# Optimization experiments

Measured on AMD Instinct MI355X. Metric: run time of the kernel, lower is better.

## Reference

```python
import jax, jax.numpy as jnp
import numpy as np

B, C, H, W = 4, 256, 64, 64
CK = C // 8  # key/query channels = 32


def setup_inputs() -> dict:
    key = jax.random.key(0)
    ks = jax.random.split(key, 5)
    s = 0.02
    return {
        "x": jax.random.normal(ks[0], (B, C, H, W), dtype=jnp.float32),
        "fw": jax.random.normal(ks[1], (CK, C), dtype=jnp.float32) * s,
        "fb": jnp.zeros((CK,), dtype=jnp.float32),
        "gw": jax.random.normal(ks[2], (CK, C), dtype=jnp.float32) * s,
        "gb": jnp.zeros((CK,), dtype=jnp.float32),
        "hw": jax.random.normal(ks[3], (C, C), dtype=jnp.float32) * s,
        "hb": jnp.zeros((C,), dtype=jnp.float32),
        "gamma": jax.random.normal(ks[4], (1,), dtype=jnp.float32),
    }


def reference(x, fw, fb, gw, gb, hw, hb, gamma):
    b, c, h, w = x.shape
    n = h * w
    xf = x.reshape(b, c, n)  # [B, C, N]
    # 1x1 convs == channel matmuls
    f = jnp.einsum('oc,bcn->bon', fw, xf) + fb[None, :, None]  # [B, CK, N]
    g = jnp.einsum('oc,bcn->bon', gw, xf) + gb[None, :, None]  # [B, CK, N]
    hv = jnp.einsum('oc,bcn->bon', hw, xf) + hb[None, :, None]  # [B, C, N]
    # attention[b,i,j] = sum_k f[b,k,i] * g[b,k,j]; softmax over j (no scaling, as in source)
    attention = jax.nn.softmax(jnp.einsum('bki,bkj->bij', f, g), axis=-1)  # [B, N, N]
    # torch.bmm(h, attention): out[b,c,m] = sum_j hv[b,c,j] * attention[b,j,m]
    sa = jnp.einsum('bcj,bjm->bcm', hv, attention).reshape(b, c, h, w)
    return gamma * sa + x
```

## Files before the change

### kernel.cpp

```cpp
#include <hip/hip_runtime.h>


typedef __bf16 bf16x4 __attribute__((ext_vector_type(4)));
typedef __bf16 bf16x8 __attribute__((ext_vector_type(8)));
typedef float  f32x4  __attribute__((ext_vector_type(4)));

static __device__ __forceinline__ bf16x8 cvt8(f32x4 lo, f32x4 hi) {
  bf16x8 r;
  r[0]=(__bf16)lo[0]; r[1]=(__bf16)lo[1]; r[2]=(__bf16)lo[2]; r[3]=(__bf16)lo[3];
  r[4]=(__bf16)hi[0]; r[5]=(__bf16)hi[1]; r[6]=(__bf16)hi[2]; r[7]=(__bf16)hi[3];
  return r;
}

__global__ __launch_bounds__(256, 2) void k_proj(
    const float* __restrict__ fw, const float* __restrict__ gw,
    const float* __restrict__ hw, const float* __restrict__ x,
    const float* __restrict__ fb, const float* __restrict__ gb,
    const float* __restrict__ hb,
    __bf16* __restrict__ gT, __bf16* __restrict__ fF, __bf16* __restrict__ hvF) {
  __shared__ __bf16 Bs[2][32][40];
  const int bid = blockIdx.x;
  const int b = (bid & 7) >> 1;
  const int n0 = (((bid >> 3) << 1) | (bid & 1)) * 32;
  const int t = threadIdx.x, mq = t >> 6, lane = t & 63, r16 = lane & 15, h = lane >> 4;
  const float* xb = x + (size_t)b * (256 * 4096);
  const float* Wp[5];
  #pragma unroll
  for (int mt = 0; mt < 5; ++mt) {
    const int wrow = mq * 80 + mt * 16 + r16;
    Wp[mt] = wrow < 32 ? (fw + wrow * 256)
           : wrow < 64 ? (gw + (wrow - 32) * 256)
                       : (hw + (wrow - 64) * 256);
  }
  const int kk = t >> 3, nc = (t & 7) * 4;
  f32x4 acc[5][2] = {};
  {
    f32x4 xv = *(const f32x4*)&xb[(size_t)kk * 4096 + n0 + nc];
    Bs[0][nc + 0][kk] = (__bf16)xv[0]; Bs[0][nc + 1][kk] = (__bf16)xv[1];
    Bs[0][nc + 2][kk] = (__bf16)xv[2]; Bs[0][nc + 3][kk] = (__bf16)xv[3];
  }
  __syncthreads();
  for (int ks = 0; ks < 8; ++ks) {
    const int cur = ks & 1;
    f32x4 xn;
    if (ks < 7) xn = *(const f32x4*)&xb[(size_t)((ks + 1) * 32 + kk) * 4096 + n0 + nc];
    bf16x8 bf0 = *(const bf16x8*)&Bs[cur][r16][h * 8];
    bf16x8 bf1 = *(const bf16x8*)&Bs[cur][16 + r16][h * 8];
    #pragma unroll
    for (int mt = 0; mt < 5; ++mt) {
      f32x4 wlo = *(const f32x4*)(Wp[mt] + ks * 32 + h * 8);
      f32x4 whi = *(const f32x4*)(Wp[mt] + ks * 32 + h * 8 + 4);
      bf16x8 af = cvt8(wlo, whi);
      acc[mt][0] = __builtin_amdgcn_mfma_f32_16x16x32_bf16(af, bf0, acc[mt][0], 0, 0, 0);
      acc[mt][1] = __builtin_amdgcn_mfma_f32_16x16x32_bf16(af, bf1, acc[mt][1], 0, 0, 0);
    }
    if (ks < 7) {
      const int nxt = cur ^ 1;
      Bs[nxt][nc + 0][kk] = (__bf16)xn[0]; Bs[nxt][nc + 1][kk] = (__bf16)xn[1];
      Bs[nxt][nc + 2][kk] = (__bf16)xn[2]; Bs[nxt][nc + 3][kk] = (__bf16)xn[3];
    }
    __syncthreads();
  }
  #pragma unroll
  for (int mt = 0; mt < 5; ++mt) {
    #pragma unroll
    for (int nt = 0; nt < 2; ++nt) {
      const int nn = n0 + nt * 16 + r16;
      const int fragn = (((b * 64 + (nn >> 6)) * 2 + ((nn >> 5) & 1)) * 2 + ((nn >> 4) & 1));
      const int jt2 = nn >> 6, jh2 = (nn >> 5) & 1;
      const int h2 = (nn >> 2) & 3, s2 = (nn >> 4) & 1, b2 = nn & 3;
      #pragma unroll
      for (int r = 0; r < 4; ++r) {
        const int row = mq * 80 + mt * 16 + h * 4 + r;
        const float bias = row < 32 ? fb[row] : (row < 64 ? gb[row - 32] : hb[row - 64]);
        float val = acc[mt][nt][r] + bias;
        if (row < 32) {
          val *= 1.44269504089f;
          const size_t off = (size_t)fragn * 512
            + (size_t)(((row >> 3) * 16 + (nn & 15)) * 8) + (row & 7);
          fF[off] = (__bf16)val;
        } else if (row < 64) {
          gT[((size_t)b * 4096 + nn) * 32 + (row - 32)] = (__bf16)val;
        } else {
          const int c = row - 64;
          const size_t off = (size_t)b * 1048576
            + (size_t)(32 * jt2 + 8 * (c >> 6) + 4 * jh2 + ((c >> 4) & 3)) * 512
            + (h2 * 16 + (c & 15)) * 8 + s2 * 4 + b2;
          hvF[off] = (__bf16)val;
        }
      }
    }
  }
}

__global__ __launch_bounds__(256) void k_pass1(const __bf16* __restrict__ gT,
                                               const __bf16* __restrict__ fF,
                                               float* __restrict__ Lp) {
  const int bid = blockIdx.x;
  const int b = (bid & 7) >> 1;
  const int sub = ((bid >> 3) << 1) | (bid & 1);
  const int ms = sub >> 6, ib = sub & 63;
  const int w = threadIdx.x >> 6, lane = threadIdx.x & 63, r16 = lane & 15, h = lane >> 4;
  const __bf16* gb_ = gT + (size_t)b * 4096 * 32;
  const int fragn = ((b * 64 + ib) * 2 + (w >> 1)) * 2 + (w & 1);
  const bf16x8 afrag = *(const bf16x8*)(fF + (size_t)fragn * 512 + lane * 8);
  const f32x4 zero = {};
  float ls0 = 0.f, ls1 = 0.f, ls2 = 0.f, ls3 = 0.f;
  for (int mt = 0; mt < 64; mt += 2) {
    const int mb = ms * 1024 + mt * 16;
    bf16x8 g0 = *(const bf16x8*)(gb_ + (size_t)(mb + r16) * 32 + h * 8);
    bf16x8 g1 = *(const bf16x8*)(gb_ + (size_t)(mb + 16 + r16) * 32 + h * 8);
    f32x4 d0 = __builtin_amdgcn_mfma_f32_16x16x32_bf16(afrag, g0, zero, 0, 0, 0);
    f32x4 d1 = __builtin_amdgcn_mfma_f32_16x16x32_bf16(afrag, g1, zero, 0, 0, 0);
    ls0 += __builtin_amdgcn_exp2f(d0[0]) + __builtin_amdgcn_exp2f(d1[0]);
    ls1 += __builtin_amdgcn_exp2f(d0[1]) + __builtin_amdgcn_exp2f(d1[1]);
    ls2 += __builtin_amdgcn_exp2f(d0[2]) + __builtin_amdgcn_exp2f(d1[2]);
    ls3 += __builtin_amdgcn_exp2f(d0[3]) + __builtin_amdgcn_exp2f(d1[3]);
  }
  #pragma unroll
  for (int off = 1; off < 16; off <<= 1) {
    ls0 += __shfl_xor(ls0, off); ls1 += __shfl_xor(ls1, off);
    ls2 += __shfl_xor(ls2, off); ls3 += __shfl_xor(ls3, off);
  }
  if (r16 == 0) {
    f32x4 o = {ls0, ls1, ls2, ls3};
    *(f32x4*)&Lp[(size_t)(b * 4 + ms) * 4096 + ib * 64 + w * 16 + h * 4] = o;
  }
}

__global__ __launch_bounds__(256) void k_wdiv(__bf16* __restrict__ hvF,
                                              const float* __restrict__ Lp) {
  const int bid = blockIdx.x;
  const int b = (bid & 7) >> 1;
  const int chunk = ((bid >> 3) << 1) | (bid & 1);
  const int t = threadIdx.x;
  const int o = chunk * 8192 + t * 32;
  const int frag = o >> 9;
  const int jh = (frag >> 2) & 1;
  const int jt = frag >> 5;
  const int l0 = (o >> 3) & 63;
  const int jb = jt * 64 + jh * 32 + ((l0 >> 4) << 2);
  const float* lp = Lp + (size_t)b * 16384 + jb;
  f32x4 La = *(const f32x4*)lp;
  La += *(const f32x4*)(lp + 4096);
  La += *(const f32x4*)(lp + 8192);
  La += *(const f32x4*)(lp + 12288);
  f32x4 Lb = *(const f32x4*)(lp + 16);
  Lb += *(const f32x4*)(lp + 16 + 4096);
  Lb += *(const f32x4*)(lp + 16 + 8192);
  Lb += *(const f32x4*)(lp + 16 + 12288);
  __bf16* p = hvF + (size_t)b * 1048576 + o;
  bf16x4 in[8];
  #pragma unroll
  for (int k = 0; k < 8; ++k) in[k] = *(const bf16x4*)(p + k * 4);
  #pragma unroll
  for (int k = 0; k < 8; ++k) {
    const f32x4 L = (k & 1) ? Lb : La;
    bf16x4 ov;
    #pragma unroll
    for (int bb = 0; bb < 4; ++bb)
      ov[bb] = (__bf16)((float)in[k][bb] / L[bb]);
    *(bf16x4*)(p + k * 4) = ov;
  }
}

__global__ __launch_bounds__(256, 2) void k_pass2(const __bf16* __restrict__ gT,
    const __bf16* __restrict__ fF, const __bf16* __restrict__ wF,
    const float* __restrict__ x, const float* __restrict__ gamma,
    float* __restrict__ out) {
  __shared__ float red[8192];
  const int bid = blockIdx.x;
  const int b = (bid & 7) >> 1;
  const int sub = ((bid >> 3) << 1) | (bid & 1);
  const int ch = sub >> 6;
  const int mblk = sub & 63;
  const int t = threadIdx.x, w = t >> 6, lane = t & 63, r16 = lane & 15, h = lane >> 4;
  const int jh = w & 1, msub = w >> 1;
  const int mbase = mblk * 64 + msub * 32;
  const __bf16* gb_ = gT + (size_t)b * 4096 * 32;
  const bf16x8 gf0 = *(const bf16x8*)(gb_ + (size_t)(mbase + r16) * 32 + h * 8);
  const bf16x8 gf1 = *(const bf16x8*)(gb_ + (size_t)(mbase + 16 + r16) * 32 + h * 8);
  const __bf16* wbase = wF + (size_t)b * 1048576 + lane * 8;
  size_t wo[8];
  #pragma unroll
  for (int ctt = 0; ctt < 8; ++ctt)
    wo[ctt] = (size_t)(8 * (2 * ch + (ctt >> 2)) + 4 * jh + (ctt & 3)) * 512;
  const __bf16* fbase = fF + ((size_t)(b * 64) * 2 + jh) * 2 * 512 + lane * 8;
  const f32x4 zero = {};

  f32x4 acc[8] = {};
  f32x4 acc2[8] = {};

  bf16x8 a0 = *(const bf16x8*)(wbase + wo[0]);
  bf16x8 a1 = *(const bf16x8*)(wbase + wo[1]);
  bf16x8 a2 = *(const bf16x8*)(wbase + wo[2]);
  bf16x8 a3 = *(const bf16x8*)(wbase + wo[3]);
  bf16x8 a4 = *(const bf16x8*)(wbase + wo[4]);
  bf16x8 a5 = *(const bf16x8*)(wbase + wo[5]);
  bf16x8 a6 = *(const bf16x8*)(wbase + wo[6]);
  bf16x8 a7 = *(const bf16x8*)(wbase + wo[7]);
  bf16x8 fq0 = *(const bf16x8*)(fbase);
  bf16x8 fq1 = *(const bf16x8*)(fbase + 512);
  bf16x8 ef0, ef1;
  {
    f32x4 d0 = __builtin_amdgcn_mfma_f32_16x16x32_bf16(fq0, gf0, zero, 0, 0, 0);
    f32x4 d1 = __builtin_amdgcn_mfma_f32_16x16x32_bf16(fq1, gf0, zero, 0, 0, 0);
    f32x4 d2 = __builtin_amdgcn_mfma_f32_16x16x32_bf16(fq0, gf1, zero, 0, 0, 0);
    f32x4 d3 = __builtin_amdgcn_mfma_f32_16x16x32_bf16(fq1, gf1, zero, 0, 0, 0);
    #pragma unroll
    for (int r = 0; r < 4; ++r) {
      ef0[r]     = (__bf16)__builtin_amdgcn_exp2f(d0[r]);
      ef0[4 + r] = (__bf16)__builtin_amdgcn_exp2f(d1[r]);
      ef1[r]     = (__bf16)__builtin_amdgcn_exp2f(d2[r]);
      ef1[4 + r] = (__bf16)__builtin_amdgcn_exp2f(d3[r]);
    }
  }
  fq0 = *(const bf16x8*)(fbase + 2048);
  fq1 = *(const bf16x8*)(fbase + 2048 + 512);

  for (int it = 0; it < 64; ++it) {
    bf16x8 pa0, pa1, pa2, pa3, pa4, pa5, pa6, pa7, nf0, nf1;
    if (it < 63) {
      const __bf16* wn = wbase + (size_t)(it + 1) * 16384;
      pa0 = *(const bf16x8*)(wn + wo[0]);
      pa1 = *(const bf16x8*)(wn + wo[1]);
      pa2 = *(const bf16x8*)(wn + wo[2]);
      pa3 = *(const bf16x8*)(wn + wo[3]);
      pa4 = *(const bf16x8*)(wn + wo[4]);
      pa5 = *(const bf16x8*)(wn + wo[5]);
      pa6 = *(const bf16x8*)(wn + wo[6]);
      pa7 = *(const bf16x8*)(wn + wo[7]);
      const __bf16* fn = fbase + (size_t)(it + 2) * 2048;
      nf0 = *(const bf16x8*)(fn);
      nf1 = *(const bf16x8*)(fn + 512);
    }
    f32x4 d0, d1, d2, d3;
    if (it < 63) {
      d0 = __builtin_amdgcn_mfma_f32_16x16x32_bf16(fq0, gf0, zero, 0, 0, 0);
      d1 = __builtin_amdgcn_mfma_f32_16x16x32_bf16(fq1, gf0, zero, 0, 0, 0);
      d2 = __builtin_amdgcn_mfma_f32_16x16x32_bf16(fq0, gf1, zero, 0, 0, 0);
      d3 = __builtin_amdgcn_mfma_f32_16x16x32_bf16(fq1, gf1, zero, 0, 0, 0);
    }
    acc[0]  = __builtin_amdgcn_mfma_f32_16x16x32_bf16(a0, ef0, acc[0],  0, 0, 0);
    acc2[0] = __builtin_amdgcn_mfma_f32_16x16x32_bf16(a0, ef1, acc2[0], 0, 0, 0);
    acc[1]  = __builtin_amdgcn_mfma_f32_16x16x32_bf16(a1, ef0, acc[1],  0, 0, 0);
    acc2[1] = __builtin_amdgcn_mfma_f32_16x16x32_bf16(a1, ef1, acc2[1], 0, 0, 0);
    acc[2]  = __builtin_amdgcn_mfma_f32_16x16x32_bf16(a2, ef0, acc[2],  0, 0, 0);
    acc2[2] = __builtin_amdgcn_mfma_f32_16x16x32_bf16(a2, ef1, acc2[2], 0, 0, 0);
    acc[3]  = __builtin_amdgcn_mfma_f32_16x16x32_bf16(a3, ef0, acc[3],  0, 0, 0);
    acc2[3] = __builtin_amdgcn_mfma_f32_16x16x32_bf16(a3, ef1, acc2[3], 0, 0, 0);
    acc[4]  = __builtin_amdgcn_mfma_f32_16x16x32_bf16(a4, ef0, acc[4],  0, 0, 0);
    acc2[4] = __builtin_amdgcn_mfma_f32_16x16x32_bf16(a4, ef1, acc2[4], 0, 0, 0);
    acc[5]  = __builtin_amdgcn_mfma_f32_16x16x32_bf16(a5, ef0, acc[5],  0, 0, 0);
    acc2[5] = __builtin_amdgcn_mfma_f32_16x16x32_bf16(a5, ef1, acc2[5], 0, 0, 0);
    acc[6]  = __builtin_amdgcn_mfma_f32_16x16x32_bf16(a6, ef0, acc[6],  0, 0, 0);
    acc2[6] = __builtin_amdgcn_mfma_f32_16x16x32_bf16(a6, ef1, acc2[6], 0, 0, 0);
    acc[7]  = __builtin_amdgcn_mfma_f32_16x16x32_bf16(a7, ef0, acc[7],  0, 0, 0);
    acc2[7] = __builtin_amdgcn_mfma_f32_16x16x32_bf16(a7, ef1, acc2[7], 0, 0, 0);
    if (it < 63) {
      #pragma unroll
      for (int r = 0; r < 4; ++r) {
        ef0[r]     = (__bf16)__builtin_amdgcn_exp2f(d0[r]);
        ef0[4 + r] = (__bf16)__builtin_amdgcn_exp2f(d1[r]);
        ef1[r]     = (__bf16)__builtin_amdgcn_exp2f(d2[r]);
        ef1[4 + r] = (__bf16)__builtin_amdgcn_exp2f(d3[r]);
      }
      a0 = pa0; a1 = pa1; a2 = pa2; a3 = pa3;
      a4 = pa4; a5 = pa5; a6 = pa6; a7 = pa7;
      fq0 = nf0; fq1 = nf1;
    }
  }

  __syncthreads();
  const int region = msub * 4096;
  if (jh == 1) {
    #pragma unroll
    for (int ct = 0; ct < 8; ++ct) {
      *(f32x4*)&red[region + ((ct * 2 + 0) * 64 + lane) * 4] = acc[ct];
      *(f32x4*)&red[region + ((ct * 2 + 1) * 64 + lane) * 4] = acc2[ct];
    }
  }
  __syncthreads();
  if (jh == 0) {
    const float gm = gamma[0];
    const float* xb = x + (size_t)b * (256 * 4096);
    float* ob = out + (size_t)b * (256 * 4096);
    #pragma unroll
    for (int ct = 0; ct < 8; ++ct) {
      #pragma unroll
      for (int mt = 0; mt < 2; ++mt) {
        f32x4 o = *(const f32x4*)&red[region + ((ct * 2 + mt) * 64 + lane) * 4];
        o += (mt == 0) ? acc[ct] : acc2[ct];
        #pragma unroll
        for (int r = 0; r < 4; ++r) {
          const int c = ch * 128 + ct * 16 + h * 4 + r;
          const size_t idx = (size_t)c * 4096 + (mbase + mt * 16 + r16);
          ob[idx] = gm * o[r] + xb[idx];
        }
      }
    }
  }
}

extern "C" void kernel_launch(void* const* d_in, const int* in_sizes, int n_in,
                              void* d_out, int out_size, void* d_ws, size_t ws_size,
                              hipStream_t stream) {
  const float* x     = (const float*)d_in[0];
  const float* fw    = (const float*)d_in[1];
  const float* fb    = (const float*)d_in[2];
  const float* gw    = (const float*)d_in[3];
  const float* gb    = (const float*)d_in[4];
  const float* hw    = (const float*)d_in[5];
  const float* hb    = (const float*)d_in[6];
  const float* gamma = (const float*)d_in[7];
  float* out = (float*)d_out;

  char* wsb = (char*)d_ws;
  __bf16* gT  = (__bf16*)(wsb);
  __bf16* fF  = (__bf16*)(wsb + 1048576);
  __bf16* hvF = (__bf16*)(wsb + 2097152);
  float*  Lp  = (float*) (wsb + 10485760);

  k_proj<<<dim3(512), dim3(256), 0, stream>>>(fw, gw, hw, x, fb, gb, hb, gT, fF, hvF);
  k_pass1<<<dim3(1024), dim3(256), 0, stream>>>(gT, fF, Lp);
  k_wdiv<<<dim3(512), dim3(256), 0, stream>>>(hvF, Lp);
  k_pass2<<<dim3(512), dim3(256), 0, stream>>>(gT, fF, hvF, x, gamma, out);
}
```

Before: 107.9 us.

## Halve pass2 query tile per wave, double grid, drop software prefetch

```diff
diff --git a/kernel.cpp b/kernel.cpp
--- a/kernel.cpp
+++ b/kernel.cpp
@@ -164,121 +164,65 @@
   }
 }
 
-__global__ __launch_bounds__(256, 2) void k_pass2(const __bf16* __restrict__ gT,
+__global__ __launch_bounds__(256, 4) void k_pass2(const __bf16* __restrict__ gT,
     const __bf16* __restrict__ fF, const __bf16* __restrict__ wF,
     const float* __restrict__ x, const float* __restrict__ gamma,
     float* __restrict__ out) {
-  __shared__ float red[8192];
+  __shared__ float red[4096];
   const int bid = blockIdx.x;
   const int b = (bid & 7) >> 1;
   const int sub = ((bid >> 3) << 1) | (bid & 1);
-  const int ch = sub >> 6;
-  const int mblk = sub & 63;
+  const int ch = sub >> 7;
+  const int mblk = sub & 127;
   const int t = threadIdx.x, w = t >> 6, lane = t & 63, r16 = lane & 15, h = lane >> 4;
   const int jh = w & 1, msub = w >> 1;
-  const int mbase = mblk * 64 + msub * 32;
+  const int mbase = mblk * 32 + msub * 16;
   const __bf16* gb_ = gT + (size_t)b * 4096 * 32;
-  const bf16x8 gf0 = *(const bf16x8*)(gb_ + (size_t)(mbase + r16) * 32 + h * 8);
-  const bf16x8 gf1 = *(const bf16x8*)(gb_ + (size_t)(mbase + 16 + r16) * 32 + h * 8);
-  const __bf16* wbase = wF + (size_t)b * 1048576 + lane * 8;
-  size_t wo[8];
-  #pragma unroll
-  for (int ctt = 0; ctt < 8; ++ctt)
-    wo[ctt] = (size_t)(8 * (2 * ch + (ctt >> 2)) + 4 * jh + (ctt & 3)) * 512;
+  const bf16x8 gf = *(const bf16x8*)(gb_ + (size_t)(mbase + r16) * 32 + h * 8);
+  const __bf16* wbase = wF + (size_t)b * 1048576
+                      + (size_t)(8 * (2 * ch) + 4 * jh) * 512 + lane * 8;
   const __bf16* fbase = fF + ((size_t)(b * 64) * 2 + jh) * 2 * 512 + lane * 8;
   const f32x4 zero = {};
 
   f32x4 acc[8] = {};
-  f32x4 acc2[8] = {};
-
-  bf16x8 a0 = *(const bf16x8*)(wbase + wo[0]);
-  bf16x8 a1 = *(const bf16x8*)(wbase + wo[1]);
-  bf16x8 a2 = *(const bf16x8*)(wbase + wo[2]);
-  bf16x8 a3 = *(const bf16x8*)(wbase + wo[3]);
-  bf16x8 a4 = *(const bf16x8*)(wbase + wo[4]);
-  bf16x8 a5 = *(const bf16x8*)(wbase + wo[5]);
-  bf16x8 a6 = *(const bf16x8*)(wbase + wo[6]);
-  bf16x8 a7 = *(const bf16x8*)(wbase + wo[7]);
-  bf16x8 fq0 = *(const bf16x8*)(fbase);
-  bf16x8 fq1 = *(const bf16x8*)(fbase + 512);
-  bf16x8 ef0, ef1;
-  {
-    f32x4 d0 = __builtin_amdgcn_mfma_f32_16x16x32_bf16(fq0, gf0, zero, 0, 0, 0);
-    f32x4 d1 = __builtin_amdgcn_mfma_f32_16x16x32_bf16(fq1, gf0, zero, 0, 0, 0);
-    f32x4 d2 = __builtin_amdgcn_mfma_f32_16x16x32_bf16(fq0, gf1, zero, 0, 0, 0);
-    f32x4 d3 = __builtin_amdgcn_mfma_f32_16x16x32_bf16(fq1, gf1, zero, 0, 0, 0);
+
+  for (int it = 0; it < 64; ++it) {
+    const __bf16* wn = wbase + (size_t)it * 16384;
+    const __bf16* fn = fbase + (size_t)it * 2048;
+    bf16x8 fq0 = *(const bf16x8*)(fn);
+    bf16x8 fq1 = *(const bf16x8*)(fn + 512);
+    bf16x8 a0 = *(const bf16x8*)(wn +    0);
+    bf16x8 a1 = *(const bf16x8*)(wn +  512);
+    bf16x8 a2 = *(const bf16x8*)(wn + 1024);
+    bf16x8 a3 = *(const bf16x8*)(wn + 1536);
+    bf16x8 a4 = *(const bf16x8*)(wn + 4096);
+    bf16x8 a5 = *(const bf16x8*)(wn + 4608);
+    bf16x8 a6 = *(const bf16x8*)(wn + 5120);
+    bf16x8 a7 = *(const bf16x8*)(wn + 5632);
+    f32x4 d0 = __builtin_amdgcn_mfma_f32_16x16x32_bf16(fq0, gf, zero, 0, 0, 0);
+    f32x4 d1 = __builtin_amdgcn_mfma_f32_16x16x32_bf16(fq1, gf, zero, 0, 0, 0);
+    bf16x8 ef;
     #pragma unroll
     for (int r = 0; r < 4; ++r) {
-      ef0[r]     = (__bf16)__builtin_amdgcn_exp2f(d0[r]);
-      ef0[4 + r] = (__bf16)__builtin_amdgcn_exp2f(d1[r]);
-      ef1[r]     = (__bf16)__builtin_amdgcn_exp2f(d2[r]);
-      ef1[4 + r] = (__bf16)__builtin_amdgcn_exp2f(d3[r]);
-    }
-  }
-  fq0 = *(const bf16x8*)(fbase + 2048);
-  fq1 = *(const bf16x8*)(fbase + 2048 + 512);
-
-  for (int it = 0; it < 64; ++it) {
-    bf16x8 pa0, pa1, pa2, pa3, pa4, pa5, pa6, pa7, nf0, nf1;
-    if (it < 63) {
-      const __bf16* wn = wbase + (size_t)(it + 1) * 16384;
-      pa0 = *(const bf16x8*)(wn + wo[0]);
-      pa1 = *(const bf16x8*)(wn + wo[1]);
-      pa2 = *(const bf16x8*)(wn + wo[2]);
-      pa3 = *(const bf16x8*)(wn + wo[3]);
-      pa4 = *(const bf16x8*)(wn + wo[4]);
-      pa5 = *(const bf16x8*)(wn + wo[5]);
-      pa6 = *(const bf16x8*)(wn + wo[6]);
-      pa7 = *(const bf16x8*)(wn + wo[7]);
-      const __bf16* fn = fbase + (size_t)(it + 2) * 2048;
-      nf0 = *(const bf16x8*)(fn);
-      nf1 = *(const bf16x8*)(fn + 512);
-    }
-    f32x4 d0, d1, d2, d3;
-    if (it < 63) {
-      d0 = __builtin_amdgcn_mfma_f32_16x16x32_bf16(fq0, gf0, zero, 0, 0, 0);
-      d1 = __builtin_amdgcn_mfma_f32_16x16x32_bf16(fq1, gf0, zero, 0, 0, 0);
-      d2 = __builtin_amdgcn_mfma_f32_16x16x32_bf16(fq0, gf1, zero, 0, 0, 0);
-      d3 = __builtin_amdgcn_mfma_f32_16x16x32_bf16(fq1, gf1, zero, 0, 0, 0);
-    }
-    acc[0]  = __builtin_amdgcn_mfma_f32_16x16x32_bf16(a0, ef0, acc[0],  0, 0, 0);
-    acc2[0] = __builtin_amdgcn_mfma_f32_16x16x32_bf16(a0, ef1, acc2[0], 0, 0, 0);
-    acc[1]  = __builtin_amdgcn_mfma_f32_16x16x32_bf16(a1, ef0, acc[1],  0, 0, 0);
-    acc2[1] = __builtin_amdgcn_mfma_f32_16x16x32_bf16(a1, ef1, acc2[1], 0, 0, 0);
-    acc[2]  = __builtin_amdgcn_mfma_f32_16x16x32_bf16(a2, ef0, acc[2],  0, 0, 0);
-    acc2[2] = __builtin_amdgcn_mfma_f32_16x16x32_bf16(a2, ef1, acc2[2], 0, 0, 0);
-    acc[3]  = __builtin_amdgcn_mfma_f32_16x16x32_bf16(a3, ef0, acc[3],  0, 0, 0);
-    acc2[3] = __builtin_amdgcn_mfma_f32_16x16x32_bf16(a3, ef1, acc2[3], 0, 0, 0);
-    acc[4]  = __builtin_amdgcn_mfma_f32_16x16x32_bf16(a4, ef0, acc[4],  0, 0, 0);
-    acc2[4] = __builtin_amdgcn_mfma_f32_16x16x32_bf16(a4, ef1, acc2[4], 0, 0, 0);
-    acc[5]  = __builtin_amdgcn_mfma_f32_16x16x32_bf16(a5, ef0, acc[5],  0, 0, 0);
-    acc2[5] = __builtin_amdgcn_mfma_f32_16x16x32_bf16(a5, ef1, acc2[5], 0, 0, 0);
-    acc[6]  = __builtin_amdgcn_mfma_f32_16x16x32_bf16(a6, ef0, acc[6],  0, 0, 0);
-    acc2[6] = __builtin_amdgcn_mfma_f32_16x16x32_bf16(a6, ef1, acc2[6], 0, 0, 0);
-    acc[7]  = __builtin_amdgcn_mfma_f32_16x16x32_bf16(a7, ef0, acc[7],  0, 0, 0);
-    acc2[7] = __builtin_amdgcn_mfma_f32_16x16x32_bf16(a7, ef1, acc2[7], 0, 0, 0);
-    if (it < 63) {
-      #pragma unroll
-      for (int r = 0; r < 4; ++r) {
-        ef0[r]     = (__bf16)__builtin_amdgcn_exp2f(d0[r]);
-        ef0[4 + r] = (__bf16)__builtin_amdgcn_exp2f(d1[r]);
-        ef1[r]     = (__bf16)__builtin_amdgcn_exp2f(d2[r]);
-        ef1[4 + r] = (__bf16)__builtin_amdgcn_exp2f(d3[r]);
-      }
-      a0 = pa0; a1 = pa1; a2 = pa2; a3 = pa3;
-      a4 = pa4; a5 = pa5; a6 = pa6; a7 = pa7;
-      fq0 = nf0; fq1 = nf1;
-    }
+      ef[r]     = (__bf16)__builtin_amdgcn_exp2f(d0[r]);
+      ef[4 + r] = (__bf16)__builtin_amdgcn_exp2f(d1[r]);
+    }
+    acc[0] = __builtin_amdgcn_mfma_f32_16x16x32_bf16(a0, ef, acc[0], 0, 0, 0);
+    acc[1] = __builtin_amdgcn_mfma_f32_16x16x32_bf16(a1, ef, acc[1], 0, 0, 0);
+    acc[2] = __builtin_amdgcn_mfma_f32_16x16x32_bf16(a2, ef, acc[2], 0, 0, 0);
+    acc[3] = __builtin_amdgcn_mfma_f32_16x16x32_bf16(a3, ef, acc[3], 0, 0, 0);
+    acc[4] = __builtin_amdgcn_mfma_f32_16x16x32_bf16(a4, ef, acc[4], 0, 0, 0);
+    acc[5] = __builtin_amdgcn_mfma_f32_16x16x32_bf16(a5, ef, acc[5], 0, 0, 0);
+    acc[6] = __builtin_amdgcn_mfma_f32_16x16x32_bf16(a6, ef, acc[6], 0, 0, 0);
+    acc[7] = __builtin_amdgcn_mfma_f32_16x16x32_bf16(a7, ef, acc[7], 0, 0, 0);
   }
 
   __syncthreads();
-  const int region = msub * 4096;
+  const int region = msub * 2048;
   if (jh == 1) {
     #pragma unroll
-    for (int ct = 0; ct < 8; ++ct) {
-      *(f32x4*)&red[region + ((ct * 2 + 0) * 64 + lane) * 4] = acc[ct];
-      *(f32x4*)&red[region + ((ct * 2 + 1) * 64 + lane) * 4] = acc2[ct];
-    }
+    for (int ct = 0; ct < 8; ++ct)
+      *(f32x4*)&red[region + (ct * 64 + lane) * 4] = acc[ct];
   }
   __syncthreads();
   if (jh == 0) {
@@ -287,16 +231,13 @@
     float* ob = out + (size_t)b * (256 * 4096);
     #pragma unroll
     for (int ct = 0; ct < 8; ++ct) {
+      f32x4 o = *(const f32x4*)&red[region + (ct * 64 + lane) * 4];
+      o += acc[ct];
       #pragma unroll
-      for (int mt = 0; mt < 2; ++mt) {
-        f32x4 o = *(const f32x4*)&red[region + ((ct * 2 + mt) * 64 + lane) * 4];
-        o += (mt == 0) ? acc[ct] : acc2[ct];
-        #pragma unroll
-        for (int r = 0; r < 4; ++r) {
-          const int c = ch * 128 + ct * 16 + h * 4 + r;
-          const size_t idx = (size_t)c * 4096 + (mbase + mt * 16 + r16);
-          ob[idx] = gm * o[r] + xb[idx];
-        }
+      for (int r = 0; r < 4; ++r) {
+        const int c = ch * 128 + ct * 16 + h * 4 + r;
+        const size_t idx = (size_t)c * 4096 + (mbase + r16);
+        ob[idx] = gm * o[r] + xb[idx];
       }
     }
   }
@@ -324,5 +265,5 @@
   k_proj<<<dim3(512), dim3(256), 0, stream>>>(fw, gw, hw, x, fb, gb, hb, gT, fF, hvF);
   k_pass1<<<dim3(1024), dim3(256), 0, stream>>>(gT, fF, Lp);
   k_wdiv<<<dim3(512), dim3(256), 0, stream>>>(hvF, Lp);
-  k_pass2<<<dim3(512), dim3(256), 0, stream>>>(gT, fF, hvF, x, gamma, out);
-}
+  k_pass2<<<dim3(1024), dim3(256), 0, stream>>>(gT, fF, hvF, x, gamma, out);
+}
```

After: 204.8 us. 1.9x slower.
